# Kernel optimization log

Measured on AMD Instinct MI355X. Metric: run time of the kernel, lower is better.

## Reference

```python
import jax, jax.numpy as jnp
import numpy as np

K = 20  # neighbors

def _bn(x, g, b, axes):
    # BatchNorm (training-mode batch statistics, eps=1e-5, biased var like torch)
    m = jnp.mean(x, axes, keepdims=True)
    v = jnp.var(x, axes, keepdims=True)
    return g * (x - m) * jax.lax.rsqrt(v + 1e-5) + b

def _edge_conv(x, W, g, b):
    # x: [B,N,d]. Dynamic kNN in feature space (self included, as in PyG knn),
    # edge feature [x_i, x_j - x_i], linear -> BN -> LeakyReLU(0.2), max over k.
    sq = jnp.sum(x * x, -1)
    d2 = sq[:, :, None] + sq[:, None, :] - 2.0 * jnp.einsum('bnd,bmd->bnm', x, x)
    _, idx = jax.lax.top_k(-d2, K)                      # [B,N,K]
    xj = jax.vmap(lambda xb, ib: xb[ib])(x, idx)        # [B,N,K,d] gather
    xi = jnp.broadcast_to(x[:, :, None, :], xj.shape)
    e = jnp.concatenate([xi, xj - xi], -1)              # [B,N,K,2d]
    h = jnp.einsum('bnke,ec->bnkc', e, W)
    h = jax.nn.leaky_relu(_bn(h, g, b, (0, 1, 2)), 0.2)
    return jnp.max(h, axis=2)                           # [B,N,C]


def setup_inputs() -> dict:
    key = jax.random.key(0)
    ks = jax.random.split(key, 24)
    B, N, NC = 16, 2048, 40
    f32 = jnp.float32
    def p(k, shape, s=0.1):
        return jax.random.normal(k, shape, f32) * s
    return {
        'pos': jax.random.normal(ks[0], (B, N, 3), f32),
        'W1': p(ks[1], (6, 64)),   'g1': jnp.ones((64,), f32),  'b1': jnp.zeros((64,), f32),
        'W2': p(ks[2], (128, 64)), 'g2': jnp.ones((64,), f32),  'b2': jnp.zeros((64,), f32),
        'W3': p(ks[3], (128, 128)),'g3': jnp.ones((128,), f32), 'b3': jnp.zeros((128,), f32),
        'Wf': p(ks[4], (256, 1024)),'gf': jnp.ones((1024,), f32),'bf': jnp.zeros((1024,), f32),
        'W4': p(ks[5], (1024, 512)), 'b4': jnp.zeros((512,), f32),
        'g4': jnp.ones((512,), f32), 'be4': jnp.zeros((512,), f32),
        'W5': p(ks[6], (512, 256)),  'b5': jnp.zeros((256,), f32),
        'g5': jnp.ones((256,), f32), 'be5': jnp.zeros((256,), f32),
        'W6': p(ks[7], (256, NC)),   'b6': jnp.zeros((NC,), f32),
    }


def reference(pos, W1, g1, b1, W2, g2, b2, W3, g3, b3, Wf, gf, bf,
              W4, b4, g4, be4, W5, b5, g5, be5, W6, b6):
    x1 = _edge_conv(pos, W1, g1, b1)    # [B,N,64]
    x2 = _edge_conv(x1, W2, g2, b2)     # [B,N,64]
    x3 = _edge_conv(x2, W3, g3, b3)     # [B,N,128]
    xc = jnp.concatenate([x1, x2, x3], -1)              # [B,N,256]
    # conv_final: 1x1 conv == per-point linear, BN over (batch, points)
    xf = jax.nn.leaky_relu(_bn(jnp.einsum('bnc,co->bno', xc, Wf), gf, bf, (0, 1)), 0.2)
    gfeat = jnp.max(xf, axis=1)                         # global max pool [B,1024]
    # classifier (Dropout treated as eval/identity)
    h = jax.nn.leaky_relu(_bn(gfeat @ W4 + b4, g4, be4, (0,)), 0.2)
    h = jax.nn.leaky_relu(_bn(h @ W5 + b5, g5, be5, (0,)), 0.2)
    return h @ W6 + b6                                  # [B,num_classes]
```

## Files before the change

### kernel.cpp

```cpp
#include <hip/hip_runtime.h>
#include <float.h>
#include <math.h>

namespace {

constexpr int NB = 16;
constexpr int NP = 2048;
constexpr int KK = 20;
constexpr int TOT = NB * NP;
constexpr int EBLK = 1024;

typedef short short8v __attribute__((ext_vector_type(8)));
typedef float f32x16 __attribute__((ext_vector_type(16)));

__device__ __forceinline__ float leaky(float v) { return fmaxf(v, 0.2f * v); }

__device__ __forceinline__ unsigned short bf16_rne(float x) {
    unsigned u = __float_as_uint(x);
    unsigned r = u + 0x7FFFu + ((u >> 16) & 1u);
    return (unsigned short)(r >> 16);
}
__device__ __forceinline__ float bf16_f(unsigned short h) {
    return __uint_as_float(((unsigned)h) << 16);
}
__device__ __forceinline__ unsigned mono_key(float d) {
    unsigned bits = __float_as_uint(d);
    return (bits & 0x80000000u) ? ~bits : (bits | 0x80000000u);
}
__device__ __forceinline__ unsigned short key16(float d) {
    return (unsigned short)(mono_key(d) >> 16);
}

__global__ __launch_bounds__(256) void pos4sq_kernel(const float* __restrict__ pos,
                                                     float* __restrict__ pos4,
                                                     float* __restrict__ sq) {
    int i = blockIdx.x * 256 + threadIdx.x;
    if (i < TOT) {
        float x = pos[i * 3 + 0], y = pos[i * 3 + 1], z = pos[i * 3 + 2];
        pos4[i * 4 + 0] = x;
        pos4[i * 4 + 1] = y;
        pos4[i * 4 + 2] = z;
        pos4[i * 4 + 3] = 0.f;
        sq[i] = x * x + y * y + z * z;
    }
}

template <int KTOT>
__global__ __launch_bounds__(256) void dist_sym16_kernel(const float* __restrict__ x, int ldx,
                                                         const float* __restrict__ sq,
                                                         int b0,
                                                         unsigned short* __restrict__ keys) {
    constexpr int KC = (KTOT < 32) ? KTOT : 32;
    constexpr int F4 = KC / 4;
    __shared__ float Ak[KC][128];
    __shared__ float Bk[KC][128];
    const int tid = threadIdx.x;
    const int tr = tid >> 4, tc = tid & 15;
    int tm = (int)((sqrtf(8.f * blockIdx.x + 1.f) - 1.f) * 0.5f);
    while ((tm + 1) * (tm + 2) / 2 <= (int)blockIdx.x) ++tm;
    while (tm * (tm + 1) / 2 > (int)blockIdx.x) --tm;
    const int tn = blockIdx.x - tm * (tm + 1) / 2;
    const int m0 = tm * 128, n0 = tn * 128;
    const int bofs = (b0 + blockIdx.y) * NP;
    const float* xb = x + (size_t)bofs * ldx;
    float acc[8][8] = {};
    for (int k0 = 0; k0 < KTOT; k0 += KC) {
        __syncthreads();
        for (int i = tid; i < 128 * F4; i += 256) {
            const int r = i / F4, c4 = i % F4;
            const int rs = r ^ ((c4 & 3) << 3);
            float4 v = *reinterpret_cast<const float4*>(xb + (size_t)(m0 + r) * ldx + k0 + c4 * 4);
            Ak[c4 * 4 + 0][rs] = v.x; Ak[c4 * 4 + 1][rs] = v.y;
            Ak[c4 * 4 + 2][rs] = v.z; Ak[c4 * 4 + 3][rs] = v.w;
        }
        for (int i = tid; i < 128 * F4; i += 256) {
            const int r = i / F4, c4 = i % F4;
            const int rs = r ^ ((c4 & 3) << 3);
            float4 v = *reinterpret_cast<const float4*>(xb + (size_t)(n0 + r) * ldx + k0 + c4 * 4);
            Bk[c4 * 4 + 0][rs] = v.x; Bk[c4 * 4 + 1][rs] = v.y;
            Bk[c4 * 4 + 2][rs] = v.z; Bk[c4 * 4 + 3][rs] = v.w;
        }
        __syncthreads();
        #pragma unroll
        for (int k = 0; k < KC; ++k) {
            const int sw = ((k >> 2) & 3) << 3;
            const int ia = (tr * 4) ^ sw;
            const int ib = (tc * 4) ^ sw;
            float4 al = *reinterpret_cast<const float4*>(&Ak[k][ia]);
            float4 ah = *reinterpret_cast<const float4*>(&Ak[k][64 + ia]);
            float4 bl = *reinterpret_cast<const float4*>(&Bk[k][ib]);
            float4 bh = *reinterpret_cast<const float4*>(&Bk[k][64 + ib]);
            float a[8] = {al.x, al.y, al.z, al.w, ah.x, ah.y, ah.z, ah.w};
            float bv[8] = {bl.x, bl.y, bl.z, bl.w, bh.x, bh.y, bh.z, bh.w};
            #pragma unroll
            for (int i = 0; i < 8; ++i)
                #pragma unroll
                for (int j = 0; j < 8; ++j)
                    acc[i][j] += a[i] * bv[j];
        }
    }
    float sa[8], sb[8];
    #pragma unroll
    for (int i = 0; i < 8; ++i) sa[i] = sq[bofs + m0 + ((i < 4) ? tr * 4 + i : 64 + tr * 4 + i - 4)];
    #pragma unroll
    for (int j = 0; j < 8; ++j) sb[j] = sq[bofs + n0 + ((j < 4) ? tc * 4 + j : 64 + tc * 4 + j - 4)];
    #pragma unroll
    for (int i = 0; i < 8; ++i) {
        const int row = (i < 4) ? tr * 4 + i : 64 + tr * 4 + i - 4;
        unsigned short* kr = keys + ((size_t)blockIdx.y * NP + m0 + row) * NP + n0;
        unsigned short kk[8];
        #pragma unroll
        for (int j = 0; j < 8; ++j) kk[j] = key16(sa[i] + sb[j] - 2.f * acc[i][j]);
        *reinterpret_cast<ushort4*>(kr + tc * 4) = make_ushort4(kk[0], kk[1], kk[2], kk[3]);
        *reinterpret_cast<ushort4*>(kr + 64 + tc * 4) = make_ushort4(kk[4], kk[5], kk[6], kk[7]);
    }
    if (tm != tn) {
        #pragma unroll
        for (int j = 0; j < 8; ++j) {
            const int col = (j < 4) ? tc * 4 + j : 64 + tc * 4 + j - 4;
            unsigned short* mr = keys + ((size_t)blockIdx.y * NP + n0 + col) * NP + m0;
            unsigned short lo4[4], hi4[4];
            #pragma unroll
            for (int i = 0; i < 4; ++i) {
                lo4[i] = key16(sa[i] + sb[j] - 2.f * acc[i][j]);
                hi4[i] = key16(sa[i + 4] + sb[j] - 2.f * acc[i + 4][j]);
            }
            *reinterpret_cast<ushort4*>(mr + tr * 4) = make_ushort4(lo4[0], lo4[1], lo4[2], lo4[3]);
            *reinterpret_cast<ushort4*>(mr + 64 + tr * 4) = make_ushort4(hi4[0], hi4[1], hi4[2], hi4[3]);
        }
    }
}

__global__ __launch_bounds__(256) void dist_mfma16_kernel(const unsigned short* __restrict__ xh,
                                                          const unsigned short* __restrict__ xl,
                                                          int ch_off,
                                                          const float* __restrict__ sq,
                                                          int b0,
                                                          unsigned short* __restrict__ keys) {
    __shared__ __align__(16) unsigned short Ah[128 * 64];
    __shared__ __align__(16) unsigned short Al[128 * 64];
    __shared__ __align__(16) unsigned short Bh[128 * 64];
    __shared__ __align__(16) unsigned short Bl[128 * 64];
    const int tid = threadIdx.x;
    const int w = tid >> 6, lane = tid & 63;
    const int wr = w >> 1, wc = w & 1;
    const int tm = blockIdx.x >> 4, tn = blockIdx.x & 15;
    const int m0 = tm * 128, n0 = tn * 128;
    const int bofs = (b0 + blockIdx.y) * NP;
    for (int i = tid; i < 1024; i += 256) {
        const int r = i >> 3, slot = i & 7;
        const int ls = r * 64 + ((slot ^ (r & 7)) << 3);
        const size_t ga = (size_t)(bofs + m0 + r) * 256 + ch_off + slot * 8;
        const size_t gb = (size_t)(bofs + n0 + r) * 256 + ch_off + slot * 8;
        *reinterpret_cast<uint4*>(&Ah[ls]) = *reinterpret_cast<const uint4*>(&xh[ga]);
        *reinterpret_cast<uint4*>(&Al[ls]) = *reinterpret_cast<const uint4*>(&xl[ga]);
        *reinterpret_cast<uint4*>(&Bh[ls]) = *reinterpret_cast<const uint4*>(&xh[gb]);
        *reinterpret_cast<uint4*>(&Bl[ls]) = *reinterpret_cast<const uint4*>(&xl[gb]);
    }
    __syncthreads();
    const int h = lane >> 5;
    const int ar0 = wr * 64 + (lane & 31), ar1 = ar0 + 32;
    const int bc0 = wc * 64 + (lane & 31), bc1 = bc0 + 32;
    f32x16 acc00 = {}, acc01 = {}, acc10 = {}, acc11 = {};
    #pragma unroll
    for (int s = 0; s < 4; ++s) {
        const int sl = s * 2 + h;
        const int ia0 = ar0 * 64 + ((sl ^ (ar0 & 7)) << 3);
        const int ia1 = ar1 * 64 + ((sl ^ (ar1 & 7)) << 3);
        const int ib0 = bc0 * 64 + ((sl ^ (bc0 & 7)) << 3);
        const int ib1 = bc1 * 64 + ((sl ^ (bc1 & 7)) << 3);
        short8v a0h = *reinterpret_cast<const short8v*>(&Ah[ia0]);
        short8v a1h = *reinterpret_cast<const short8v*>(&Ah[ia1]);
        short8v a0l = *reinterpret_cast<const short8v*>(&Al[ia0]);
        short8v a1l = *reinterpret_cast<const short8v*>(&Al[ia1]);
        short8v b0h = *reinterpret_cast<const short8v*>(&Bh[ib0]);
        short8v b1h = *reinterpret_cast<const short8v*>(&Bh[ib1]);
        short8v b0l = *reinterpret_cast<const short8v*>(&Bl[ib0]);
        short8v b1l = *reinterpret_cast<const short8v*>(&Bl[ib1]);
        acc00 = __builtin_amdgcn_mfma_f32_32x32x16_bf16(a0h, b0h, acc00, 0, 0, 0);
        acc01 = __builtin_amdgcn_mfma_f32_32x32x16_bf16(a0h, b1h, acc01, 0, 0, 0);
        acc10 = __builtin_amdgcn_mfma_f32_32x32x16_bf16(a1h, b0h, acc10, 0, 0, 0);
        acc11 = __builtin_amdgcn_mfma_f32_32x32x16_bf16(a1h, b1h, acc11, 0, 0, 0);
        acc00 = __builtin_amdgcn_mfma_f32_32x32x16_bf16(a0h, b0l, acc00, 0, 0, 0);
        acc01 = __builtin_amdgcn_mfma_f32_32x32x16_bf16(a0h, b1l, acc01, 0, 0, 0);
        acc10 = __builtin_amdgcn_mfma_f32_32x32x16_bf16(a1h, b0l, acc10, 0, 0, 0);
        acc11 = __builtin_amdgcn_mfma_f32_32x32x16_bf16(a1h, b1l, acc11, 0, 0, 0);
        acc00 = __builtin_amdgcn_mfma_f32_32x32x16_bf16(a0l, b0h, acc00, 0, 0, 0);
        acc01 = __builtin_amdgcn_mfma_f32_32x32x16_bf16(a0l, b1h, acc01, 0, 0, 0);
        acc10 = __builtin_amdgcn_mfma_f32_32x32x16_bf16(a1l, b0h, acc10, 0, 0, 0);
        acc11 = __builtin_amdgcn_mfma_f32_32x32x16_bf16(a1l, b1h, acc11, 0, 0, 0);
    }
    const int colg0 = n0 + bc0;
    const int colg1 = n0 + bc1;
    const float sqc0 = sq[bofs + colg0];
    const float sqc1 = sq[bofs + colg1];
    unsigned short* kb = keys + (size_t)blockIdx.y * NP * NP;
    #pragma unroll
    for (int ai = 0; ai < 2; ++ai) {
        const f32x16& A0 = ai ? acc10 : acc00;
        const f32x16& A1 = ai ? acc11 : acc01;
        #pragma unroll
        for (int q = 0; q < 4; ++q) {
            const int rbase = wr * 64 + ai * 32 + 8 * q + 4 * h;
            float sr[4];
            #pragma unroll
            for (int j = 0; j < 4; ++j) sr[j] = sq[bofs + m0 + rbase + j];
            ushort4 s0, s1;
            s0.x = key16(sr[0] + sqc0 - 2.f * A0[q * 4 + 0]);
            s0.y = key16(sr[1] + sqc0 - 2.f * A0[q * 4 + 1]);
            s0.z = key16(sr[2] + sqc0 - 2.f * A0[q * 4 + 2]);
            s0.w = key16(sr[3] + sqc0 - 2.f * A0[q * 4 + 3]);
            s1.x = key16(sr[0] + sqc1 - 2.f * A1[q * 4 + 0]);
            s1.y = key16(sr[1] + sqc1 - 2.f * A1[q * 4 + 1]);
            s1.z = key16(sr[2] + sqc1 - 2.f * A1[q * 4 + 2]);
            s1.w = key16(sr[3] + sqc1 - 2.f * A1[q * 4 + 3]);
            *reinterpret_cast<ushort4*>(&kb[(size_t)colg0 * NP + m0 + rbase]) = s0;
            *reinterpret_cast<ushort4*>(&kb[(size_t)colg1 * NP + m0 + rbase]) = s1;
        }
    }
}

template <int D>
__global__ __launch_bounds__(256) void knn_sr_kernel(const unsigned short* __restrict__ keys,
                                                     int b0,
                                                     const float* __restrict__ xf, int ldx,
                                                     const float* __restrict__ sq,
                                                     int* __restrict__ idx_out) {
    constexpr int D4 = D / 4;
    __shared__ int scand[4][64];
    const int tid = threadIdx.x;
    const int w = tid >> 6, lane = tid & 63;
    const int ql = blockIdx.x * 4 + w;
    const int bc = ql / NP;
    const int bofs = (b0 + bc) * NP;
    const int q = b0 * NP + ql;
    const unsigned* kr = reinterpret_cast<const unsigned*>(keys) + (size_t)ql * (NP / 2);

    unsigned kv[16];
    #pragma unroll
    for (int v = 0; v < 16; ++v) kv[v] = kr[v * 64 + lane];

    unsigned lmn = 0xFFFFu;
    #pragma unroll
    for (int v = 0; v < 16; ++v) {
        lmn = min(lmn, kv[v] & 0xFFFFu);
        lmn = min(lmn, kv[v] >> 16);
    }
    unsigned lo = lmn, hi = lmn;
    #pragma unroll
    for (int s = 1; s < 64; s <<= 1) {
        unsigned tl = __shfl_xor(lo, s);
        unsigned th = __shfl_xor(hi, s);
        lo = min(lo, tl);
        hi = max(hi, th);
    }
    while (lo < hi) {
        unsigned mid = (lo + hi) >> 1;
        int c = __popcll(__ballot(lmn <= mid));
        if (c >= KK) hi = mid; else lo = mid + 1;
    }
    const unsigned T = min(lo + 6u, 0xFFFFu);

    unsigned nl = 0;
    #pragma unroll
    for (int v = 0; v < 16; ++v) {
        nl += ((kv[v] & 0xFFFFu) <= T) ? 1u : 0u;
        nl += ((kv[v] >> 16) <= T) ? 1u : 0u;
    }
    unsigned sc = nl;
    #pragma unroll
    for (int s = 1; s < 64; s <<= 1) {
        unsigned t2 = __shfl_up(sc, s);
        if (lane >= s) sc += t2;
    }
    const int cnt = (int)__shfl(sc, 63);
    unsigned off = sc - nl;
    #pragma unroll
    for (int v = 0; v < 16; ++v) {
        if ((kv[v] & 0xFFFFu) <= T) { if (off < 64u) scand[w][off] = bofs + (v * 64 + lane) * 2; ++off; }
        if ((kv[v] >> 16) <= T)     { if (off < 64u) scand[w][off] = bofs + (v * 64 + lane) * 2 + 1; ++off; }
    }

    float4 qv[D4];
    const float4* xq4 = reinterpret_cast<const float4*>(xf + (size_t)q * ldx);
    #pragma unroll
    for (int k = 0; k < D4; ++k) qv[k] = xq4[k];
    const float sqq = sq[q];
    int* op = idx_out + (size_t)q * KK;

    if (cnt <= 64) {
        const int cidx = (lane < cnt) ? scand[w][lane] : -1;
        unsigned key = 0xFFFFFFFFu;
        if (cidx >= 0) {
            const float4* xc4 = reinterpret_cast<const float4*>(xf + (size_t)cidx * ldx);
            float acc = 0.f;
            #pragma unroll
            for (int k = 0; k < D4; ++k) {
                float4 c = xc4[k];
                acc += qv[k].x * c.x; acc += qv[k].y * c.y;
                acc += qv[k].z * c.z; acc += qv[k].w * c.w;
            }
            key = mono_key(sqq + sq[cidx] - 2.f * acc);
        }
        unsigned klo = key, khi = key;
        #pragma unroll
        for (int s = 1; s < 64; s <<= 1) {
            unsigned tl = __shfl_xor(klo, s);
            unsigned th = __shfl_xor(khi, s);
            klo = min(klo, tl);
            khi = max(khi, th);
        }
        while (klo < khi) {
            unsigned mid = klo + ((khi - klo) >> 1);
            int c = __popcll(__ballot(key <= mid));
            if (c >= KK) khi = mid; else klo = mid + 1;
        }
        const unsigned Tx = klo;
        unsigned long long blt = __ballot(key < Tx);
        const int strict = __popcll(blt);
        if (key < Tx) {
            int o = __popcll(blt & ((1ull << lane) - 1ull));
            op[o] = cidx;
        }
        const int rem = KK - strict;
        bool eq = (key == Tx) && (cidx >= 0);
        bool done = false;
        for (int t = 0; t < rem; ++t) {
            int v = (eq && !done) ? cidx : 0x7FFFFFFF;
            #pragma unroll
            for (int s = 1; s < 64; s <<= 1) v = min(v, __shfl_xor(v, s));
            if (eq && !done && cidx == v) { op[strict + t] = cidx; done = true; }
        }
    } else {
        unsigned keysr[32];
        for (int u = 0; u < 32; ++u) {
            const int c = bofs + u * 64 + lane;
            const float4* xc4 = reinterpret_cast<const float4*>(xf + (size_t)c * ldx);
            float acc = 0.f;
            #pragma unroll
            for (int k = 0; k < D4; ++k) {
                float4 cv = xc4[k];
                acc += qv[k].x * cv.x; acc += qv[k].y * cv.y;
                acc += qv[k].z * cv.z; acc += qv[k].w * cv.w;
            }
            keysr[u] = mono_key(sqq + sq[c] - 2.f * acc);
        }
        unsigned lmn2 = 0xFFFFFFFFu;
        #pragma unroll
        for (int u = 0; u < 32; ++u) lmn2 = min(lmn2, keysr[u]);
        unsigned M2 = lmn2, lo2 = lmn2;
        #pragma unroll
        for (int s = 1; s < 64; s <<= 1) {
            unsigned tM = __shfl_xor(M2, s);
            unsigned tl = __shfl_xor(lo2, s);
            M2 = max(M2, tM);
            lo2 = min(lo2, tl);
        }
        unsigned hi2 = M2;
        while (lo2 < hi2) {
            unsigned mid = lo2 + ((hi2 - lo2) >> 1);
            int c = 0;
            #pragma unroll
            for (int u = 0; u < 32; ++u)
                c += __popcll(__ballot(keysr[u] <= mid));
            if (c >= KK) hi2 = mid; else lo2 = mid + 1;
        }
        const unsigned Tx = lo2;
        unsigned nl2 = 0;
        #pragma unroll
        for (int u = 0; u < 32; ++u) nl2 += (keysr[u] < Tx) ? 1u : 0u;
        unsigned sc2 = nl2;
        #pragma unroll
        for (int s = 1; s < 64; s <<= 1) {
            unsigned t2 = __shfl_up(sc2, s);
            if (lane >= s) sc2 += t2;
        }
        unsigned cstrict = __shfl(sc2, 63);
        unsigned o = sc2 - nl2;
        #pragma unroll
        for (int u = 0; u < 32; ++u) {
            if (keysr[u] < Tx) { op[o] = bofs + u * 64 + lane; ++o; }
        }
        int rem = KK - (int)cstrict;
        int ebase = (int)cstrict;
        #pragma unroll
        for (int u = 0; u < 32; ++u) {
            if (rem > 0) {
                bool eq = (keysr[u] == Tx);
                unsigned long long bm = __ballot(eq);
                int before = __popcll(bm & ((1ull << lane) - 1ull));
                if (eq && before < rem) op[ebase + before] = bofs + u * 64 + lane;
                int take = __popcll(bm);
                if (take > rem) take = rem;
                ebase += take;
                rem -= take;
            }
        }
    }
}

__global__ __launch_bounds__(256) void wt_build_kernel(const float* __restrict__ W,
                                                       float* __restrict__ Wt,
                                                       int D, int Dp, int C) {
    int i = blockIdx.x * 256 + threadIdx.x;
    if (i < 2 * C * Dp) {
        int c = i / Dp, j = i % Dp;
        float v = 0.f;
        if (j < D) {
            v = (c < C) ? (W[j * C + c] - W[(D + j) * C + c])
                        : W[(D + j) * C + (c - C)];
        }
        Wt[i] = v;
    }
}

template <int NJ4, int C2>
__global__ __launch_bounds__(256) void xw_gemm_kernel(const float* __restrict__ x, int ldx,
                                                      const float* __restrict__ Wt,
                                                      float* __restrict__ bx) {
    constexpr int PG = 256 / C2;
    constexpr int PTS = 16 / PG;
    __shared__ float4 Xs[16][NJ4];
    const int tid = threadIdx.x;
    const int p0 = blockIdx.x * 16;
    for (int i = tid; i < 16 * NJ4; i += 256) {
        int r = i / NJ4, j4 = i % NJ4;
        Xs[r][j4] = *reinterpret_cast<const float4*>(x + (size_t)(p0 + r) * ldx + j4 * 4);
    }
    __syncthreads();
    const int c = tid % C2, pg = tid / C2;
    const float4* wrow = reinterpret_cast<const float4*>(Wt + (size_t)c * (NJ4 * 4));
    float acc[PTS];
    #pragma unroll
    for (int u = 0; u < PTS; ++u) acc[u] = 0.f;
    #pragma unroll
    for (int j4 = 0; j4 < NJ4; ++j4) {
        float4 w4 = wrow[j4];
        #pragma unroll
        for (int u = 0; u < PTS; ++u) {
            float4 x4 = Xs[pg * PTS + u][j4];
            acc[u] += x4.x * w4.x + x4.y * w4.y + x4.z * w4.z + x4.w * w4.w;
        }
    }
    #pragma unroll
    for (int u = 0; u < PTS; ++u)
        bx[(size_t)(p0 + pg * PTS + u) * C2 + c] = acc[u];
}

template <int C>
__global__ __launch_bounds__(256) void edge_pass_kernel(const float* __restrict__ bx,
                                                        const int* __restrict__ idx,
                                                        float* __restrict__ psum,
                                                        float* __restrict__ psum2,
                                                        float* __restrict__ mmax,
                                                        float* __restrict__ mmin) {
    constexpr int PT = 256 / C;
    constexpr int C2 = 2 * C;
    __shared__ int sidx[PT][KK];
    __shared__ float red[256];
    const int tid = threadIdx.x;
    const int c = tid % C;
    const int pl = tid / C;
    float s1 = 0.f, s2 = 0.f;
    const int NT = TOT / PT;
    for (int t = blockIdx.x; t < NT; t += EBLK) {
        const int p0 = t * PT;
        __syncthreads();
        if (tid < PT * KK) sidx[tid / KK][tid % KK] = idx[(size_t)p0 * KK + tid];
        __syncthreads();
        const int p = p0 + pl;
        const float bv = bx[(size_t)p * C2 + c];
        float A = 0.f, Q = 0.f, M = -FLT_MAX, mn = FLT_MAX;
        #pragma unroll
        for (int k = 0; k < KK; ++k) {
            float v = bx[(size_t)sidx[pl][k] * C2 + C + c];
            A += v; Q += v * v; M = fmaxf(M, v); mn = fminf(mn, v);
        }
        s1 += (float)KK * bv + A;
        s2 += (float)KK * bv * bv + 2.f * bv * A + Q;
        mmax[(size_t)p * C + c] = bv + M;
        mmin[(size_t)p * C + c] = bv + mn;
    }
    red[tid] = s1;
    __syncthreads();
    if (tid < C) {
        float v = red[tid];
        #pragma unroll
        for (int u = 1; u < PT; ++u) v += red[tid + u * C];
        psum[(size_t)blockIdx.x * C + tid] = v;
    }
    __syncthreads();
    red[tid] = s2;
    __syncthreads();
    if (tid < C) {
        float v = red[tid];
        #pragma unroll
        for (int u = 1; u < PT; ++u) v += red[tid + u * C];
        psum2[(size_t)blockIdx.x * C + tid] = v;
    }
}

__global__ __launch_bounds__(256) void bn_reduce_kernel(
        const float* __restrict__ psum, const float* __restrict__ psum2,
        int npart, int C, const float* __restrict__ g, const float* __restrict__ bb,
        float inv_cnt, float* __restrict__ alpha, float* __restrict__ beta) {
    const int c = blockIdx.x;
    const int tid = threadIdx.x;
    __shared__ float r1[256], r2[256];
    float s1 = 0.f, s2 = 0.f;
    for (int i = tid; i < npart; i += 256) {
        s1 += psum[(size_t)i * C + c];
        s2 += psum2[(size_t)i * C + c];
    }
    r1[tid] = s1; r2[tid] = s2;
    __syncthreads();
    for (int s = 128; s > 0; s >>= 1) {
        if (tid < s) { r1[tid] += r1[tid + s]; r2[tid] += r2[tid + s]; }
        __syncthreads();
    }
    if (tid == 0) {
        float mean = r1[0] * inv_cnt;
        float var = r2[0] * inv_cnt - mean * mean;
        float a = g[c] * rsqrtf(var + 1e-5f);
        alpha[c] = a;
        beta[c] = bb[c] - mean * a;
    }
}

template <int C>
__global__ __launch_bounds__(256) void edge_finalize_kernel(const float* __restrict__ mmax,
                                                            const float* __restrict__ mmin,
                                                            const float* __restrict__ alpha,
                                                            const float* __restrict__ beta,
                                                            float* __restrict__ xcf, int ldf,
                                                            unsigned short* __restrict__ xch,
                                                            unsigned short* __restrict__ xcl,
                                                            int ch_off,
                                                            float* __restrict__ sq_out) {
    constexpr int CQ = C / 4;
    __shared__ float red[256];
    const int tid = threadIdx.x;
    int i4 = blockIdx.x * 256 + tid;
    float4 o = make_float4(0.f, 0.f, 0.f, 0.f);
    int p = 0;
    if (i4 < TOT * CQ) {
        int cq; p = i4 / CQ; cq = i4 - p * CQ;
        float4 M4 = reinterpret_cast<const float4*>(mmax)[i4];
        float4 m4 = reinterpret_cast<const float4*>(mmin)[i4];
        float4 a4 = reinterpret_cast<const float4*>(alpha)[cq];
        float4 b4 = reinterpret_cast<const float4*>(beta)[cq];
        o.x = leaky(a4.x * (a4.x >= 0.f ? M4.x : m4.x) + b4.x);
        o.y = leaky(a4.y * (a4.y >= 0.f ? M4.y : m4.y) + b4.y);
        o.z = leaky(a4.z * (a4.z >= 0.f ? M4.z : m4.z) + b4.z);
        o.w = leaky(a4.w * (a4.w >= 0.f ? M4.w : m4.w) + b4.w);
        if (xcf)
            *reinterpret_cast<float4*>(xcf + (size_t)p * ldf + cq * 4) = o;
        ushort4 hh, ll;
        hh.x = bf16_rne(o.x); ll.x = bf16_rne(o.x - bf16_f(hh.x));
        hh.y = bf16_rne(o.y); ll.y = bf16_rne(o.y - bf16_f(hh.y));
        hh.z = bf16_rne(o.z); ll.z = bf16_rne(o.z - bf16_f(hh.z));
        hh.w = bf16_rne(o.w); ll.w = bf16_rne(o.w - bf16_f(hh.w));
        const size_t oo = (size_t)p * 256 + ch_off + cq * 4;
        *reinterpret_cast<ushort4*>(xch + oo) = hh;
        *reinterpret_cast<ushort4*>(xcl + oo) = ll;
    }
    if (sq_out) {
        red[tid] = o.x * o.x + o.y * o.y + o.z * o.z + o.w * o.w;
        __syncthreads();
        if ((tid & (CQ - 1)) == 0) {
            float s = red[tid];
            #pragma unroll
            for (int u = 1; u < CQ; ++u) s += red[tid + u];
            sq_out[p] = s;
        }
    }
}

__global__ __launch_bounds__(256) void wfhl_build_kernel(const float* __restrict__ Wf,
                                                         unsigned short* __restrict__ wfh,
                                                         unsigned short* __restrict__ wfl) {
    int i = blockIdx.x * 256 + threadIdx.x;
    if (i < 256 * 1024) {
        int e = i / 1024, o = i - e * 1024;
        float v = Wf[i];
        unsigned short h = bf16_rne(v);
        wfh[(size_t)o * 256 + e] = h;
        wfl[(size_t)o * 256 + e] = bf16_rne(v - bf16_f(h));
    }
}

__global__ __launch_bounds__(256) void fc_mfma_kernel(const unsigned short* __restrict__ xch,
                                                      const unsigned short* __restrict__ xcl,
                                                      const unsigned short* __restrict__ wfh,
                                                      const unsigned short* __restrict__ wfl,
                                                      float* __restrict__ psum,
                                                      float* __restrict__ psum2,
                                                      float* __restrict__ pmax,
                                                      float* __restrict__ pmin) {
    __shared__ __align__(16) unsigned short Ah[128 * 64];
    __shared__ __align__(16) unsigned short Al[128 * 64];
    __shared__ __align__(16) unsigned short Bh[128 * 64];
    __shared__ __align__(16) unsigned short Bl[128 * 64];
    const int tid = threadIdx.x;
    const int w = tid >> 6, lane = tid & 63;
    const int wr = w >> 1, wc = w & 1;
    const int pt = blockIdx.x, ct = blockIdx.y;
    f32x16 acc00 = {}, acc01 = {}, acc10 = {}, acc11 = {};
    for (int kc = 0; kc < 4; ++kc) {
        const int k0 = kc * 64;
        __syncthreads();
        for (int i = tid; i < 1024; i += 256) {
            const int r = i >> 3, slot = i & 7;
            const int ls = r * 64 + ((slot ^ (r & 7)) << 3);
            const size_t ga = (size_t)(pt * 128 + r) * 256 + k0 + slot * 8;
            const size_t gb = (size_t)(ct * 128 + r) * 256 + k0 + slot * 8;
            *reinterpret_cast<uint4*>(&Ah[ls]) = *reinterpret_cast<const uint4*>(&xch[ga]);
            *reinterpret_cast<uint4*>(&Al[ls]) = *reinterpret_cast<const uint4*>(&xcl[ga]);
            *reinterpret_cast<uint4*>(&Bh[ls]) = *reinterpret_cast<const uint4*>(&wfh[gb]);
            *reinterpret_cast<uint4*>(&Bl[ls]) = *reinterpret_cast<const uint4*>(&wfl[gb]);
        }
        __syncthreads();
        const int h = lane >> 5;
        const int ar0 = wr * 64 + (lane & 31), ar1 = ar0 + 32;
        const int bc0 = wc * 64 + (lane & 31), bc1 = bc0 + 32;
        #pragma unroll
        for (int s = 0; s < 4; ++s) {
            const int sl = s * 2 + h;
            const int ia0 = ar0 * 64 + ((sl ^ (ar0 & 7)) << 3);
            const int ia1 = ar1 * 64 + ((sl ^ (ar1 & 7)) << 3);
            const int ib0 = bc0 * 64 + ((sl ^ (bc0 & 7)) << 3);
            const int ib1 = bc1 * 64 + ((sl ^ (bc1 & 7)) << 3);
            short8v a0h = *reinterpret_cast<const short8v*>(&Ah[ia0]);
            short8v a1h = *reinterpret_cast<const short8v*>(&Ah[ia1]);
            short8v a0l = *reinterpret_cast<const short8v*>(&Al[ia0]);
            short8v a1l = *reinterpret_cast<const short8v*>(&Al[ia1]);
            short8v b0h = *reinterpret_cast<const short8v*>(&Bh[ib0]);
            short8v b1h = *reinterpret_cast<const short8v*>(&Bh[ib1]);
            short8v b0l = *reinterpret_cast<const short8v*>(&Bl[ib0]);
            short8v b1l = *reinterpret_cast<const short8v*>(&Bl[ib1]);
            acc00 = __builtin_amdgcn_mfma_f32_32x32x16_bf16(a0h, b0h, acc00, 0, 0, 0);
            acc01 = __builtin_amdgcn_mfma_f32_32x32x16_bf16(a0h, b1h, acc01, 0, 0, 0);
            acc10 = __builtin_amdgcn_mfma_f32_32x32x16_bf16(a1h, b0h, acc10, 0, 0, 0);
            acc11 = __builtin_amdgcn_mfma_f32_32x32x16_bf16(a1h, b1h, acc11, 0, 0, 0);
            acc00 = __builtin_amdgcn_mfma_f32_32x32x16_bf16(a0h, b0l, acc00, 0, 0, 0);
            acc01 = __builtin_amdgcn_mfma_f32_32x32x16_bf16(a0h, b1l, acc01, 0, 0, 0);
            acc10 = __builtin_amdgcn_mfma_f32_32x32x16_bf16(a1h, b0l, acc10, 0, 0, 0);
            acc11 = __builtin_amdgcn_mfma_f32_32x32x16_bf16(a1h, b1l, acc11, 0, 0, 0);
            acc00 = __builtin_amdgcn_mfma_f32_32x32x16_bf16(a0l, b0h, acc00, 0, 0, 0);
            acc01 = __builtin_amdgcn_mfma_f32_32x32x16_bf16(a0l, b1h, acc01, 0, 0, 0);
            acc10 = __builtin_amdgcn_mfma_f32_32x32x16_bf16(a1l, b0h, acc10, 0, 0, 0);
            acc11 = __builtin_amdgcn_mfma_f32_32x32x16_bf16(a1l, b1h, acc11, 0, 0, 0);
        }
    }
    float* red = reinterpret_cast<float*>(Ah);
    __syncthreads();
    #pragma unroll
    for (int fc = 0; fc < 2; ++fc) {
        float s1 = 0.f, s2 = 0.f, mx = -FLT_MAX, mn = FLT_MAX;
        #pragma unroll
        for (int e = 0; e < 16; ++e) {
            float v0 = (fc == 0) ? acc00[e] : acc01[e];
            float v1 = (fc == 0) ? acc10[e] : acc11[e];
            s1 += v0 + v1;
            s2 += v0 * v0 + v1 * v1;
            mx = fmaxf(mx, fmaxf(v0, v1));
            mn = fminf(mn, fminf(v0, v1));
        }
        s1 += __shfl_xor(s1, 32);
        s2 += __shfl_xor(s2, 32);
        mx = fmaxf(mx, __shfl_xor(mx, 32));
        mn = fminf(mn, __shfl_xor(mn, 32));
        if (lane < 32) {
            const int ch = wc * 64 + fc * 32 + lane;
            float4 st; st.x = s1; st.y = s2; st.z = mx; st.w = mn;
            *reinterpret_cast<float4*>(&red[(wr * 128 + ch) * 4]) = st;
        }
    }
    __syncthreads();
    if (tid < 128) {
        float4 s0 = *reinterpret_cast<const float4*>(&red[tid * 4]);
        float4 s1 = *reinterpret_cast<const float4*>(&red[(128 + tid) * 4]);
        const size_t go = (size_t)pt * 1024 + ct * 128 + tid;
        psum[go]  = s0.x + s1.x;
        psum2[go] = s0.y + s1.y;
        pmax[go]  = fmaxf(s0.z, s1.z);
        pmin[go]  = fminf(s0.w, s1.w);
    }
}

__global__ __launch_bounds__(256) void gfeat_final_kernel(const float* __restrict__ pmax,
                                                          const float* __restrict__ pmin,
                                                          const float* __restrict__ alpha,
                                                          const float* __restrict__ beta,
                                                          float* __restrict__ gfeat) {
    int i = blockIdx.x * 256 + threadIdx.x;
    if (i < NB * 1024) {
        int b = i >> 10, c = i & 1023;
        float mx = -FLT_MAX, mn = FLT_MAX;
        for (int j = 0; j < 16; ++j) {
            size_t o = (size_t)(b * 16 + j) * 1024 + c;
            mx = fmaxf(mx, pmax[o]);
            mn = fminf(mn, pmin[o]);
        }
        float a = alpha[c];
        gfeat[i] = leaky(a * (a >= 0.f ? mx : mn) + beta[c]);
    }
}

template <int CHUNK>
__global__ __launch_bounds__(256) void skinny_gemm_kernel(const float* __restrict__ A,
                                                          const float* __restrict__ W,
                                                          float* __restrict__ part,
                                                          int K, int N) {
    __shared__ float Asub[4][16][CHUNK];
    const int tid = threadIdx.x;
    const int g = tid >> 6, lane = tid & 63;
    const int c = blockIdx.x * 64 + lane;
    const int ks = blockIdx.y * 4 + g;
    const int e0 = ks * CHUNK;
    for (int i = lane; i < 16 * CHUNK; i += 64) {
        const int m = i / CHUNK, el = i - m * CHUNK;
        Asub[g][m][el] = A[(size_t)m * K + e0 + el];
    }
    if (c < N) {
        float acc[16];
        #pragma unroll
        for (int m = 0; m < 16; ++m) acc[m] = 0.f;
        #pragma unroll 4
        for (int el = 0; el < CHUNK; ++el) {
            float w = W[(size_t)(e0 + el) * N + c];
            #pragma unroll
            for (int m = 0; m < 16; ++m) acc[m] += Asub[g][m][el] * w;
        }
        #pragma unroll
        for (int m = 0; m < 16; ++m)
            part[((size_t)ks * 16 + m) * N + c] = acc[m];
    }
}

__global__ __launch_bounds__(256) void fin_kernel(const float* __restrict__ part,
                                                  int S, int N,
                                                  const float* __restrict__ bias,
                                                  const float* __restrict__ g,
                                                  const float* __restrict__ bb,
                                                  int do_bn,
                                                  float* __restrict__ out, int Nout) {
    int c = blockIdx.x * 256 + threadIdx.x;
    if (c >= N) return;
    float z[16];
    #pragma unroll
    for (int m = 0; m < 16; ++m) z[m] = bias[c];
    for (int s = 0; s < S; ++s)
        #pragma unroll
        for (int m = 0; m < 16; ++m) z[m] += part[((size_t)s * 16 + m) * N + c];
    if (do_bn) {
        float s1 = 0.f, s2 = 0.f;
        #pragma unroll
        for (int m = 0; m < 16; ++m) { s1 += z[m]; s2 += z[m] * z[m]; }
        float mean = s1 * (1.f / 16.f);
        float var = s2 * (1.f / 16.f) - mean * mean;
        float a = g[c] * rsqrtf(var + 1e-5f);
        float be = bb[c] - mean * a;
        #pragma unroll
        for (int m = 0; m < 16; ++m) out[(size_t)m * N + c] = leaky(a * z[m] + be);
    } else {
        if (c < Nout)
            #pragma unroll
            for (int m = 0; m < 16; ++m) out[(size_t)m * Nout + c] = z[m];
    }
}

static void run_knn_l1(const float* x, const float* sq, unsigned short* keys16, int CB,
                       int* idx, hipStream_t stream) {
    for (int b0 = 0; b0 < NB; b0 += CB) {
        dim3 g(136, CB);
        dist_sym16_kernel<4><<<g, 256, 0, stream>>>(x, 4, sq, b0, keys16);
        knn_sr_kernel<4><<<CB * NP / 4, 256, 0, stream>>>(keys16, b0, x, 4, sq, idx);
    }
}

static void run_knn_feat(const unsigned short* xh, const unsigned short* xl, int ch_off,
                         const float* xf, const float* sq, unsigned short* keys16, int CB,
                         int* idx, hipStream_t stream) {
    for (int b0 = 0; b0 < NB; b0 += CB) {
        dim3 g(256, CB);
        dist_mfma16_kernel<<<g, 256, 0, stream>>>(xh, xl, ch_off, sq, b0, keys16);
        knn_sr_kernel<64><<<CB * NP / 4, 256, 0, stream>>>(keys16, b0, xf, 128, sq, idx);
    }
}

}

extern "C" void kernel_launch(void* const* d_in, const int* in_sizes, int n_in,
                              void* d_out, int out_size, void* d_ws, size_t ws_size,
                              hipStream_t stream) {
    (void)in_sizes; (void)n_in; (void)out_size;
    const float* pos = (const float*)d_in[0];
    const float* W1  = (const float*)d_in[1];
    const float* g1  = (const float*)d_in[2];
    const float* b1  = (const float*)d_in[3];
    const float* W2  = (const float*)d_in[4];
    const float* g2  = (const float*)d_in[5];
    const float* b2  = (const float*)d_in[6];
    const float* W3  = (const float*)d_in[7];
    const float* g3  = (const float*)d_in[8];
    const float* b3  = (const float*)d_in[9];
    const float* Wf  = (const float*)d_in[10];
    const float* gf  = (const float*)d_in[11];
    const float* bf  = (const float*)d_in[12];
    const float* W4  = (const float*)d_in[13];
    const float* b4  = (const float*)d_in[14];
    const float* g4  = (const float*)d_in[15];
    const float* be4 = (const float*)d_in[16];
    const float* W5  = (const float*)d_in[17];
    const float* b5  = (const float*)d_in[18];
    const float* g5  = (const float*)d_in[19];
    const float* be5 = (const float*)d_in[20];
    const float* W6  = (const float*)d_in[21];
    const float* b6  = (const float*)d_in[22];
    float* out = (float*)d_out;

    float* ws = (float*)d_ws;
    size_t off = 0;
    int*   idx    = (int*)ws;      off += (size_t)TOT * KK;
    float* pos4   = ws + off;      off += (size_t)TOT * 4;
    float* sq     = ws + off;      off += (size_t)TOT;
    float* Wt     = ws + off;      off += 256 * 64;
    float* basexw = ws + off;      off += (size_t)TOT * 256;
    float* mmax   = ws + off;      off += (size_t)TOT * 128;
    float* mmin   = ws + off;      off += (size_t)TOT * 128;
    float* xc12   = ws + off;      off += (size_t)TOT * 128;
    unsigned short* xch = (unsigned short*)(ws + off); off += (size_t)TOT * 128;
    unsigned short* xcl = (unsigned short*)(ws + off); off += (size_t)TOT * 128;
    unsigned short* wfh = (unsigned short*)(ws + off); off += (size_t)1024 * 128;
    unsigned short* wfl = (unsigned short*)(ws + off); off += (size_t)1024 * 128;
    float* psum   = ws + off;      off += (size_t)512 * 1024;
    float* psum2  = ws + off;      off += (size_t)512 * 1024;
    float* pmax   = ws + off;      off += (size_t)512 * 1024;
    float* pmin   = ws + off;      off += (size_t)512 * 1024;
    float* alpha  = ws + off;      off += 1024;
    float* beta   = ws + off;      off += 1024;
    float* gfeat  = ws + off;      off += NB * 1024;
    float* part   = ws + off;      off += 8 * 16 * 512;
    float* h4     = ws + off;      off += NB * 512;
    float* h5     = ws + off;      off += NB * 256;
    unsigned short* keys16 = (unsigned short*)(ws + off);
    const size_t avail = (ws_size > off * 4) ? (ws_size - off * 4) : 0;
    const size_t per_batch = (size_t)NP * NP * 2;
    int CB = 1;
    for (int cb : {8, 4, 2}) {
        if ((size_t)cb * per_batch <= avail) { CB = cb; break; }
    }

    const int npts_blk = (TOT + 255) / 256;

    pos4sq_kernel<<<npts_blk, 256, 0, stream>>>(pos, pos4, sq);
    run_knn_l1(pos4, sq, keys16, CB, idx, stream);
    wt_build_kernel<<<2, 256, 0, stream>>>(W1, Wt, 3, 4, 64);
    xw_gemm_kernel<1, 128><<<TOT / 16, 256, 0, stream>>>(pos4, 4, Wt, basexw);
    edge_pass_kernel<64><<<EBLK, 256, 0, stream>>>(basexw, idx, psum, psum2, mmax, mmin);
    bn_reduce_kernel<<<64, 256, 0, stream>>>(psum, psum2, EBLK, 64, g1, b1,
                                             1.f / (float)(TOT * KK), alpha, beta);
    edge_finalize_kernel<64><<<TOT * 16 / 256, 256, 0, stream>>>(
        mmax, mmin, alpha, beta, xc12 + 0, 128, xch, xcl, 0, sq);

    run_knn_feat(xch, xcl, 0, xc12 + 0, sq, keys16, CB, idx, stream);
    wt_build_kernel<<<32, 256, 0, stream>>>(W2, Wt, 64, 64, 64);
    xw_gemm_kernel<16, 128><<<TOT / 16, 256, 0, stream>>>(xc12 + 0, 128, Wt, basexw);
    edge_pass_kernel<64><<<EBLK, 256, 0, stream>>>(basexw, idx, psum, psum2, mmax, mmin);
    bn_reduce_kernel<<<64, 256, 0, stream>>>(psum, psum2, EBLK, 64, g2, b2,
                                             1.f / (float)(TOT * KK), alpha, beta);
    edge_finalize_kernel<64><<<TOT * 16 / 256, 256, 0, stream>>>(
        mmax, mmin, alpha, beta, xc12 + 64, 128, xch, xcl, 64, sq);

    run_knn_feat(xch, xcl, 64, xc12 + 64, sq, keys16, CB, idx, stream);
    wt_build_kernel<<<64, 256, 0, stream>>>(W3, Wt, 64, 64, 128);
    xw_gemm_kernel<16, 256><<<TOT / 16, 256, 0, stream>>>(xc12 + 64, 128, Wt, basexw);
    edge_pass_kernel<128><<<EBLK, 256, 0, stream>>>(basexw, idx, psum, psum2, mmax, mmin);
    bn_reduce_kernel<<<128, 256, 0, stream>>>(psum, psum2, EBLK, 128, g3, b3,
                                              1.f / (float)(TOT * KK), alpha, beta);
    edge_finalize_kernel<128><<<TOT * 32 / 256, 256, 0, stream>>>(
        mmax, mmin, alpha, beta, nullptr, 0, xch, xcl, 128, nullptr);

    wfhl_build_kernel<<<1024, 256, 0, stream>>>(Wf, wfh, wfl);
    {
        dim3 g(TOT / 128, 8, 1);
        fc_mfma_kernel<<<g, 256, 0, stream>>>(xch, xcl, wfh, wfl, psum, psum2, pmax, pmin);
    }
    bn_reduce_kernel<<<1024, 256, 0, stream>>>(psum, psum2, 256, 1024, gf, bf,
                                               1.f / (float)TOT, alpha, beta);
    gfeat_final_kernel<<<64, 256, 0, stream>>>(pmax, pmin, alpha, beta, gfeat);

    skinny_gemm_kernel<128><<<dim3(8, 2), 256, 0, stream>>>(gfeat, W4, part, 1024, 512);
    fin_kernel<<<2, 256, 0, stream>>>(part, 8, 512, b4, g4, be4, 1, h4, 512);
    skinny_gemm_kernel<64><<<dim3(4, 2), 256, 0, stream>>>(h4, W5, part, 512, 256);
    fin_kernel<<<1, 256, 0, stream>>>(part, 8, 256, b5, g5, be5, 1, h5, 256);
    skinny_gemm_kernel<32><<<dim3(1, 2), 256, 0, stream>>>(h5, W6, part, 256, 40);
    fin_kernel<<<1, 256, 0, stream>>>(part, 8, 40, b6, nullptr, nullptr, 0, out, 40);
}
```

Baseline: 742.8 us.

## Fuse layer-1 kNN distance and selection into one kernel, drop key matrix

```diff
diff --git a/kernel.cpp b/kernel.cpp
--- a/kernel.cpp
+++ b/kernel.cpp
@@ -45,88 +45,147 @@
     }
 }
 
-template <int KTOT>
-__global__ __launch_bounds__(256) void dist_sym16_kernel(const float* __restrict__ x, int ldx,
-                                                         const float* __restrict__ sq,
-                                                         int b0,
-                                                         unsigned short* __restrict__ keys) {
-    constexpr int KC = (KTOT < 32) ? KTOT : 32;
-    constexpr int F4 = KC / 4;
-    __shared__ float Ak[KC][128];
-    __shared__ float Bk[KC][128];
+__global__ __launch_bounds__(256) void knn_l1_fused_kernel(const float* __restrict__ x,
+                                                           const float* __restrict__ sq,
+                                                           int* __restrict__ idx_out) {
+    __shared__ float4 xs[NP];
+    __shared__ float sqs[NP];
+    __shared__ int scand[4][64];
     const int tid = threadIdx.x;
-    const int tr = tid >> 4, tc = tid & 15;
-    int tm = (int)((sqrtf(8.f * blockIdx.x + 1.f) - 1.f) * 0.5f);
-    while ((tm + 1) * (tm + 2) / 2 <= (int)blockIdx.x) ++tm;
-    while (tm * (tm + 1) / 2 > (int)blockIdx.x) --tm;
-    const int tn = blockIdx.x - tm * (tm + 1) / 2;
-    const int m0 = tm * 128, n0 = tn * 128;
-    const int bofs = (b0 + blockIdx.y) * NP;
-    const float* xb = x + (size_t)bofs * ldx;
-    float acc[8][8] = {};
-    for (int k0 = 0; k0 < KTOT; k0 += KC) {
-        __syncthreads();
-        for (int i = tid; i < 128 * F4; i += 256) {
-            const int r = i / F4, c4 = i % F4;
-            const int rs = r ^ ((c4 & 3) << 3);
-            float4 v = *reinterpret_cast<const float4*>(xb + (size_t)(m0 + r) * ldx + k0 + c4 * 4);
-            Ak[c4 * 4 + 0][rs] = v.x; Ak[c4 * 4 + 1][rs] = v.y;
-            Ak[c4 * 4 + 2][rs] = v.z; Ak[c4 * 4 + 3][rs] = v.w;
-        }
-        for (int i = tid; i < 128 * F4; i += 256) {
-            const int r = i / F4, c4 = i % F4;
-            const int rs = r ^ ((c4 & 3) << 3);
-            float4 v = *reinterpret_cast<const float4*>(xb + (size_t)(n0 + r) * ldx + k0 + c4 * 4);
-            Bk[c4 * 4 + 0][rs] = v.x; Bk[c4 * 4 + 1][rs] = v.y;
-            Bk[c4 * 4 + 2][rs] = v.z; Bk[c4 * 4 + 3][rs] = v.w;
-        }
-        __syncthreads();
-        #pragma unroll
-        for (int k = 0; k < KC; ++k) {
-            const int sw = ((k >> 2) & 3) << 3;
-            const int ia = (tr * 4) ^ sw;
-            const int ib = (tc * 4) ^ sw;
-            float4 al = *reinterpret_cast<const float4*>(&Ak[k][ia]);
-            float4 ah = *reinterpret_cast<const float4*>(&Ak[k][64 + ia]);
-            float4 bl = *reinterpret_cast<const float4*>(&Bk[k][ib]);
-            float4 bh = *reinterpret_cast<const float4*>(&Bk[k][64 + ib]);
-            float a[8] = {al.x, al.y, al.z, al.w, ah.x, ah.y, ah.z, ah.w};
-            float bv[8] = {bl.x, bl.y, bl.z, bl.w, bh.x, bh.y, bh.z, bh.w};
-            #pragma unroll
-            for (int i = 0; i < 8; ++i)
+    const int w = tid >> 6, lane = tid & 63;
+    const int b = blockIdx.x >> 7;
+    const int chunk = blockIdx.x & 127;
+    const int bofs = b * NP;
+    for (int i = tid; i < NP; i += 256) {
+        xs[i] = *reinterpret_cast<const float4*>(x + (size_t)(bofs + i) * 4);
+        sqs[i] = sq[bofs + i];
+    }
+    __syncthreads();
+    for (int qi = 0; qi < 4; ++qi) {
+        const int qloc = chunk * 16 + w * 4 + qi;
+        const float4 qv = xs[qloc];
+        const float sqq = sqs[qloc];
+        unsigned keys[32];
+        unsigned lmn = 0xFFFFFFFFu;
+        #pragma unroll
+        for (int u = 0; u < 32; ++u) {
+            const int m = u * 64 + lane;
+            float4 c = xs[m];
+            float dot = qv.x * c.x + qv.y * c.y + qv.z * c.z + qv.w * c.w;
+            keys[u] = mono_key(sqq + sqs[m] - 2.f * dot);
+            lmn = min(lmn, keys[u]);
+        }
+        unsigned lo = lmn, hi = lmn;
+        #pragma unroll
+        for (int s = 1; s < 64; s <<= 1) {
+            lo = min(lo, __shfl_xor(lo, s));
+            hi = max(hi, __shfl_xor(hi, s));
+        }
+        while (lo < hi) {
+            unsigned mid = lo + ((hi - lo) >> 1);
+            int c = __popcll(__ballot(lmn <= mid));
+            if (c >= KK) hi = mid; else lo = mid + 1;
+        }
+        const unsigned B = lo;
+        unsigned nl = 0;
+        #pragma unroll
+        for (int u = 0; u < 32; ++u) nl += (keys[u] <= B) ? 1u : 0u;
+        unsigned sc = nl;
+        #pragma unroll
+        for (int s = 1; s < 64; s <<= 1) {
+            unsigned t2 = __shfl_up(sc, s);
+            if (lane >= s) sc += t2;
+        }
+        const int cnt = (int)__shfl(sc, 63);
+        unsigned off = sc - nl;
+        #pragma unroll
+        for (int u = 0; u < 32; ++u) {
+            if (keys[u] <= B) { if (off < 64u) scand[w][off] = u * 64 + lane; ++off; }
+        }
+        int* op = idx_out + (size_t)(bofs + qloc) * KK;
+        if (cnt <= 64) {
+            const int cl = (lane < cnt) ? scand[w][lane] : -1;
+            unsigned key = 0xFFFFFFFFu;
+            if (cl >= 0) {
+                float4 c = xs[cl];
+                float dot = qv.x * c.x + qv.y * c.y + qv.z * c.z + qv.w * c.w;
+                key = mono_key(sqq + sqs[cl] - 2.f * dot);
+            }
+            unsigned klo = key, khi = key;
+            #pragma unroll
+            for (int s = 1; s < 64; s <<= 1) {
+                klo = min(klo, __shfl_xor(klo, s));
+                khi = max(khi, __shfl_xor(khi, s));
+            }
+            while (klo < khi) {
+                unsigned mid = klo + ((khi - klo) >> 1);
+                int c = __popcll(__ballot(key <= mid));
+                if (c >= KK) khi = mid; else klo = mid + 1;
+            }
+            const unsigned Tx = klo;
+            unsigned long long blt = __ballot(key < Tx);
+            const int strict = __popcll(blt);
+            if (key < Tx) {
+                int o = __popcll(blt & ((1ull << lane) - 1ull));
+                op[o] = bofs + cl;
+            }
+            const int rem = KK - strict;
+            bool eq = (key == Tx) && (cl >= 0);
+            bool done = false;
+            for (int t = 0; t < rem; ++t) {
+                int v = (eq && !done) ? cl : 0x7FFFFFFF;
                 #pragma unroll
-                for (int j = 0; j < 8; ++j)
-                    acc[i][j] += a[i] * bv[j];
-        }
-    }
-    float sa[8], sb[8];
-    #pragma unroll
-    for (int i = 0; i < 8; ++i) sa[i] = sq[bofs + m0 + ((i < 4) ? tr * 4 + i : 64 + tr * 4 + i - 4)];
-    #pragma unroll
-    for (int j = 0; j < 8; ++j) sb[j] = sq[bofs + n0 + ((j < 4) ? tc * 4 + j : 64 + tc * 4 + j - 4)];
-    #pragma unroll
-    for (int i = 0; i < 8; ++i) {
-        const int row = (i < 4) ? tr * 4 + i : 64 + tr * 4 + i - 4;
-        unsigned short* kr = keys + ((size_t)blockIdx.y * NP + m0 + row) * NP + n0;
-        unsigned short kk[8];
-        #pragma unroll
-        for (int j = 0; j < 8; ++j) kk[j] = key16(sa[i] + sb[j] - 2.f * acc[i][j]);
-        *reinterpret_cast<ushort4*>(kr + tc * 4) = make_ushort4(kk[0], kk[1], kk[2], kk[3]);
-        *reinterpret_cast<ushort4*>(kr + 64 + tc * 4) = make_ushort4(kk[4], kk[5], kk[6], kk[7]);
-    }
-    if (tm != tn) {
-        #pragma unroll
-        for (int j = 0; j < 8; ++j) {
-            const int col = (j < 4) ? tc * 4 + j : 64 + tc * 4 + j - 4;
-            unsigned short* mr = keys + ((size_t)blockIdx.y * NP + n0 + col) * NP + m0;
-            unsigned short lo4[4], hi4[4];
-            #pragma unroll
-            for (int i = 0; i < 4; ++i) {
-                lo4[i] = key16(sa[i] + sb[j] - 2.f * acc[i][j]);
-                hi4[i] = key16(sa[i + 4] + sb[j] - 2.f * acc[i + 4][j]);
-            }
-            *reinterpret_cast<ushort4*>(mr + tr * 4) = make_ushort4(lo4[0], lo4[1], lo4[2], lo4[3]);
-            *reinterpret_cast<ushort4*>(mr + 64 + tr * 4) = make_ushort4(hi4[0], hi4[1], hi4[2], hi4[3]);
+                for (int s = 1; s < 64; s <<= 1) v = min(v, __shfl_xor(v, s));
+                if (eq && !done && cl == v) { op[strict + t] = bofs + cl; done = true; }
+            }
+        } else {
+            unsigned lo2 = lmn, hi2 = 0;
+            #pragma unroll
+            for (int u = 0; u < 32; ++u) hi2 = max(hi2, keys[u]);
+            #pragma unroll
+            for (int s = 1; s < 64; s <<= 1) {
+                lo2 = min(lo2, __shfl_xor(lo2, s));
+                hi2 = max(hi2, __shfl_xor(hi2, s));
+            }
+            while (lo2 < hi2) {
+                unsigned mid = lo2 + ((hi2 - lo2) >> 1);
+                int c = 0;
+                #pragma unroll
+                for (int u = 0; u < 32; ++u)
+                    c += __popcll(__ballot(keys[u] <= mid));
+                if (c >= KK) hi2 = mid; else lo2 = mid + 1;
+            }
+            const unsigned Tx = lo2;
+            unsigned nl2 = 0;
+            #pragma unroll
+            for (int u = 0; u < 32; ++u) nl2 += (keys[u] < Tx) ? 1u : 0u;
+            unsigned sc2 = nl2;
+            #pragma unroll
+            for (int s = 1; s < 64; s <<= 1) {
+                unsigned t2 = __shfl_up(sc2, s);
+                if (lane >= s) sc2 += t2;
+            }
+            unsigned cstrict = __shfl(sc2, 63);
+            unsigned o = sc2 - nl2;
+            #pragma unroll
+            for (int u = 0; u < 32; ++u) {
+                if (keys[u] < Tx) { op[o] = bofs + u * 64 + lane; ++o; }
+            }
+            int rem = KK - (int)cstrict;
+            int ebase = (int)cstrict;
+            #pragma unroll
+            for (int u = 0; u < 32; ++u) {
+                if (rem > 0) {
+                    bool eq = (keys[u] == Tx);
+                    unsigned long long bm = __ballot(eq);
+                    int before = __popcll(bm & ((1ull << lane) - 1ull));
+                    if (eq && before < rem) op[ebase + before] = bofs + u * 64 + lane;
+                    int take = __popcll(bm);
+                    if (take > rem) take = rem;
+                    ebase += take;
+                    rem -= take;
+                }
+            }
         }
     }
 }
@@ -249,10 +308,8 @@
     unsigned lo = lmn, hi = lmn;
     #pragma unroll
     for (int s = 1; s < 64; s <<= 1) {
-        unsigned tl = __shfl_xor(lo, s);
-        unsigned th = __shfl_xor(hi, s);
-        lo = min(lo, tl);
-        hi = max(hi, th);
+        lo = min(lo, __shfl_xor(lo, s));
+        hi = max(hi, __shfl_xor(hi, s));
     }
     while (lo < hi) {
         unsigned mid = (lo + hi) >> 1;
@@ -305,10 +362,8 @@
         unsigned klo = key, khi = key;
         #pragma unroll
         for (int s = 1; s < 64; s <<= 1) {
-            unsigned tl = __shfl_xor(klo, s);
-            unsigned th = __shfl_xor(khi, s);
-            klo = min(klo, tl);
-            khi = max(khi, th);
+            klo = min(klo, __shfl_xor(klo, s));
+            khi = max(khi, __shfl_xor(khi, s));
         }
         while (klo < khi) {
             unsigned mid = klo + ((khi - klo) >> 1);
@@ -770,15 +825,6 @@
     }
 }
 
-static void run_knn_l1(const float* x, const float* sq, unsigned short* keys16, int CB,
-                       int* idx, hipStream_t stream) {
-    for (int b0 = 0; b0 < NB; b0 += CB) {
-        dim3 g(136, CB);
-        dist_sym16_kernel<4><<<g, 256, 0, stream>>>(x, 4, sq, b0, keys16);
-        knn_sr_kernel<4><<<CB * NP / 4, 256, 0, stream>>>(keys16, b0, x, 4, sq, idx);
-    }
-}
-
 static void run_knn_feat(const unsigned short* xh, const unsigned short* xl, int ch_off,
                          const float* xf, const float* sq, unsigned short* keys16, int CB,
                          int* idx, hipStream_t stream) {
@@ -855,7 +901,7 @@
     const int npts_blk = (TOT + 255) / 256;
 
     pos4sq_kernel<<<npts_blk, 256, 0, stream>>>(pos, pos4, sq);
-    run_knn_l1(pos4, sq, keys16, CB, idx, stream);
+    knn_l1_fused_kernel<<<TOT / 16, 256, 0, stream>>>(pos4, sq, idx);
     wt_build_kernel<<<2, 256, 0, stream>>>(W1, Wt, 3, 4, 64);
     xw_gemm_kernel<1, 128><<<TOT / 16, 256, 0, stream>>>(pos4, 4, Wt, basexw);
     edge_pass_kernel<64><<<EBLK, 256, 0, stream>>>(basexw, idx, psum, psum2, mmax, mmin);
```

After: 858.9 us. 15.6% more time.
